# Performance work log

Measured on AMD Instinct MI355X. Metric: run time of the kernel, lower is better.

## Reference

```python
import jax, jax.numpy as jnp
import numpy as np

N = 50000      # nodes
E = 800000     # edges (avg degree 16)
IN = 100       # in_channels (hard-coded LayerNorm(100))
H = 128        # hidden_channels
G = 512        # num graphs in batch
C = 2          # num_classes
EPS = 1e-5     # LayerNorm eps (torch default)


def setup_inputs() -> dict:
    key = jax.random.key(0)
    ks = jax.random.split(key, 12)
    x = jax.random.normal(ks[0], (N, IN), dtype=jnp.float32)
    edge_index = jax.random.randint(ks[1], (2, E), 0, N, dtype=jnp.int64)
    edge_weight = jax.random.uniform(ks[2], (E,), dtype=jnp.float32)
    batch = jnp.sort(jax.random.randint(ks[3], (N,), 0, G, dtype=jnp.int64))
    # LayerNorm params (identity init, as torch)
    ln_g0, ln_b0 = jnp.ones((IN,), jnp.float32), jnp.zeros((IN,), jnp.float32)
    ln_g1, ln_b1 = jnp.ones((H,), jnp.float32), jnp.zeros((H,), jnp.float32)
    ln_g2, ln_b2 = jnp.ones((H,), jnp.float32), jnp.zeros((H,), jnp.float32)
    # GCNConv weights (glorot-ish scale) and biases
    W0 = jax.random.normal(ks[4], (IN, H), jnp.float32) / np.float32(np.sqrt(IN))
    b0 = jnp.zeros((H,), jnp.float32)
    W1 = jax.random.normal(ks[5], (H, H), jnp.float32) / np.float32(np.sqrt(H))
    b1 = jnp.zeros((H,), jnp.float32)
    W2 = jax.random.normal(ks[6], (H, H), jnp.float32) / np.float32(np.sqrt(H))
    b2 = jnp.zeros((H,), jnp.float32)
    # Final classifier
    Wlin = jax.random.normal(ks[7], (H, C), jnp.float32) / np.float32(np.sqrt(H))
    blin = jnp.zeros((C,), jnp.float32)
    return {"x": x, "edge_index": edge_index, "edge_weight": edge_weight,
            "batch": batch,
            "ln_g0": ln_g0, "ln_b0": ln_b0, "ln_g1": ln_g1, "ln_b1": ln_b1,
            "ln_g2": ln_g2, "ln_b2": ln_b2,
            "W0": W0, "b0": b0, "W1": W1, "b1": b1, "W2": W2, "b2": b2,
            "Wlin": Wlin, "blin": blin}


def _layernorm(h, g, b):
    m = jnp.mean(h, axis=-1, keepdims=True)
    v = jnp.mean(jnp.square(h - m), axis=-1, keepdims=True)
    return (h - m) * jax.lax.rsqrt(v + EPS) * g + b


def _gcn_conv(h, W, b, src, dst, edge_weight):
    # GCNConv(normalize=False): linear transform, edge gather scaled by
    # edge_weight, scatter-add to destination nodes, plus bias.
    hW = h @ W                                  # [N, H]
    msg = hW[src] * edge_weight[:, None]        # [E, H]
    agg = jax.ops.segment_sum(msg, dst, num_segments=N)  # [N, H]
    return agg + b


def reference(x, edge_index, edge_weight, batch,
              ln_g0, ln_b0, ln_g1, ln_b1, ln_g2, ln_b2,
              W0, b0, W1, b1, W2, b2, Wlin, blin):
    src, dst = edge_index[0], edge_index[1]
    layers = [(ln_g0, ln_b0, W0, b0), (ln_g1, ln_b1, W1, b1), (ln_g2, ln_b2, W2, b2)]
    h = x
    for (g, bb, W, cb) in layers:
        h = _layernorm(h, g, bb)
        h = _gcn_conv(h, W, cb, src, dst, edge_weight)
        h = jax.nn.relu(h)  # dropout is identity in eval mode
    # global mean pool over graphs
    sums = jax.ops.segment_sum(h, batch, num_segments=G)                       # [G, H]
    cnt = jax.ops.segment_sum(jnp.ones((N, 1), h.dtype), batch, num_segments=G)
    pooled = sums / jnp.maximum(cnt, 1.0)
    return pooled @ Wlin + blin  # [G, C]
```

## Files before the change

### kernel.cpp

```cpp
#include <hip/hip_runtime.h>
#include <hip/hip_bf16.h>

#define NN 50000
#define NE 800000
#define NG 512
#define HD 128
#define EPS 1e-5f
#define NB ((NN + 255) / 256)
#define L1B NB
#define EPB 4096
#define NL1 ((NE + EPB - 1) / EPB)

typedef __attribute__((ext_vector_type(8))) short short8;
typedef __attribute__((ext_vector_type(4))) float f32x4;

__global__ __launch_bounds__(256) void k_zero(int* __restrict__ deg,
                                              float* __restrict__ pooled) {
    const int i = blockIdx.x * 256 + threadIdx.x;
    if (i < NN) deg[i] = 0;
    if (i < NG * HD) pooled[i] = 0.f;
}

__global__ __launch_bounds__(256) void k_hist(const int* __restrict__ dstv,
                                              int* __restrict__ deg, int E) {
    int e = blockIdx.x * 256 + threadIdx.x;
    if (e < E) atomicAdd(&deg[dstv[e]], 1);
}

__global__ __launch_bounds__(256) void k_blksum(const int* __restrict__ deg,
                                                int* __restrict__ bsum) {
    __shared__ int red[4];
    const int i = blockIdx.x * 256 + threadIdx.x;
    int v = (i < NN) ? deg[i] : 0;
#pragma unroll
    for (int off = 32; off; off >>= 1) v += __shfl_down(v, off);
    const int lane = threadIdx.x & 63, w = threadIdx.x >> 6;
    if (lane == 0) red[w] = v;
    __syncthreads();
    if (threadIdx.x == 0) bsum[blockIdx.x] = red[0] + red[1] + red[2] + red[3];
}

__global__ __launch_bounds__(256) void k_scan_bsum(const int* __restrict__ bsum,
                                                   int* __restrict__ boff) {
    __shared__ int s[256];
    const int t = threadIdx.x;
    const int v = (t < NB) ? bsum[t] : 0;
    s[t] = v;
    __syncthreads();
    for (int off = 1; off < 256; off <<= 1) {
        int u = (t >= off) ? s[t - off] : 0;
        __syncthreads();
        s[t] += u;
        __syncthreads();
    }
    if (t < NB) boff[t] = s[t] - v;
}

__global__ __launch_bounds__(256) void k_scan_final(const int* __restrict__ deg,
                                                    const int* __restrict__ boff,
                                                    int* __restrict__ row_ptr) {
    __shared__ int s[256];
    const int t = threadIdx.x;
    const int i = blockIdx.x * 256 + t;
    const int v = (i < NN) ? deg[i] : 0;
    s[t] = v;
    __syncthreads();
    for (int off = 1; off < 256; off <<= 1) {
        int u = (t >= off) ? s[t - off] : 0;
        __syncthreads();
        s[t] += u;
        __syncthreads();
    }
    const int ex = boff[blockIdx.x] + s[t] - v;
    if (i < NN) row_ptr[i] = ex;
    if (i == NN - 1) row_ptr[NN] = ex + v;
}

__global__ __launch_bounds__(256) void k_initgc(const int* __restrict__ row_ptr,
                                                int* __restrict__ gcursor) {
    const int b = threadIdx.x;
    if (b < L1B) {
        int d = b << 8;
        gcursor[b] = row_ptr[(d < NN) ? d : NN];
    }
}

__global__ __launch_bounds__(256) void k_binL1(const int* __restrict__ srcv,
                                               const int* __restrict__ dstv,
                                               const float* __restrict__ ewt,
                                               int* __restrict__ gcursor,
                                               int2* __restrict__ stage, int E) {
    __shared__ int hist[L1B], lstart[L1B], gbase[L1B], lcur[L1B];
    __shared__ int s[256];
    __shared__ int2 lsort[EPB];
    const int t  = threadIdx.x;
    const int e0 = blockIdx.x * EPB;
    const int e1 = (e0 + EPB < E) ? (e0 + EPB) : E;
    for (int i = t; i < L1B; i += 256) hist[i] = 0;
    __syncthreads();
    for (int e = e0 + t; e < e1; e += 256)
        atomicAdd(&hist[dstv[e] >> 8], 1);
    __syncthreads();
    {
        const int v = (t < L1B) ? hist[t] : 0;
        s[t] = v;
        __syncthreads();
        for (int off = 1; off < 256; off <<= 1) {
            int u = (t >= off) ? s[t - off] : 0;
            __syncthreads();
            s[t] += u;
            __syncthreads();
        }
        if (t < L1B) {
            const int ex = s[t] - v;
            lstart[t] = ex;
            lcur[t]   = ex;
            gbase[t]  = v ? atomicAdd(&gcursor[t], v) : 0;
        }
    }
    __syncthreads();
    for (int e = e0 + t; e < e1; e += 256) {
        const int d = dstv[e];
        const int r = atomicAdd(&lcur[d >> 8], 1);
        lsort[r] = make_int2((d << 16) | srcv[e], __float_as_int(ewt[e]));
    }
    __syncthreads();
    const int n = e1 - e0;
    for (int i = t; i < n; i += 256) {
        const int2 el = lsort[i];
        const unsigned b = ((unsigned)el.x) >> 24;
        stage[gbase[b] + (i - lstart[b])] = el;
    }
}

__global__ __launch_bounds__(256) void k_binL2(const int2* __restrict__ stage,
                                               const int* __restrict__ row_ptr,
                                               int2* __restrict__ cw) {
    __shared__ int cur[256];
    const int t  = threadIdx.x;
    const int d0 = blockIdx.x << 8;
    const int nd = (NN - d0 < 256) ? (NN - d0) : 256;
    if (t < nd) cur[t] = row_ptr[d0 + t];
    __syncthreads();
    const int base = row_ptr[d0];
    const int end  = row_ptr[d0 + nd];
    for (int i = base + t; i < end; i += 256) {
        const int2 el = stage[i];
        const unsigned dst = ((unsigned)el.x) >> 16;
        const int p = atomicAdd(&cur[dst - d0], 1);
        cw[p] = make_int2(el.x & 0xFFFF, el.y);
    }
}

__global__ __launch_bounds__(256) void k_wpack(const float* __restrict__ W0,
                                               const float* __restrict__ W1,
                                               const float* __restrict__ W2,
                                               __hip_bfloat16* __restrict__ bp) {
    const int tg    = blockIdx.x * 256 + threadIdx.x;
    const int layer = tg >> 11;
    const int f     = tg & 2047;
    const int tile  = f >> 8, kk = (f >> 6) & 3, lane = f & 63;
    const int col   = tile * 16 + (lane & 15);
    const int kbase = kk * 32 + ((lane >> 4) << 3);
    const float* W  = (layer == 0) ? W0 : (layer == 1) ? W1 : W2;
    const int Klim  = (layer == 0) ? 100 : 128;
    alignas(16) __hip_bfloat16 o[8];
#pragma unroll
    for (int j = 0; j < 8; ++j) {
        const int k = kbase + j;
        o[j] = __float2bfloat16((k < Klim) ? W[(size_t)k * HD + col] : 0.f);
    }
    *(float4*)&bp[(size_t)tg * 8] = *(const float4*)o;
}

template <int K>
__global__ __launch_bounds__(256, 3) void k_ln_gemm(const float* __restrict__ hin,
                                                    const float* __restrict__ g,
                                                    const float* __restrict__ b,
                                                    const __hip_bfloat16* __restrict__ bp,
                                                    __hip_bfloat16* __restrict__ hwb) {
    constexpr int SK   = K + 4;
    constexpr int ROWS = 64;
    __shared__ float hs[ROWS][SK];
    __shared__ __hip_bfloat16 hb[ROWS][136];
    const int t  = threadIdx.x;
    const int r0 = blockIdx.x * ROWS;

    {
        const float4* src4 = (const float4*)(hin + (size_t)r0 * K);
        const int valid_rows = (NN - r0 < ROWS) ? (NN - r0) : ROWS;
        const int maxf = valid_rows * K;
        constexpr int NV = ROWS * K / 4;
        for (int i = t; i < NV; i += 256) {
            int f = i * 4;
            float4 v = (f < maxf) ? src4[i] : make_float4(0.f, 0.f, 0.f, 0.f);
            int r = f / K, k = f - r * K;
            *(float4*)&hs[r][k] = v;
        }
    }
    __syncthreads();

    {
        const int row = t >> 2, l = t & 3;
        float s = 0.f, s2 = 0.f;
        for (int k = l; k < K; k += 4) { float v = hs[row][k]; s += v; s2 += v * v; }
        s  += __shfl_xor(s, 1);  s2 += __shfl_xor(s2, 1);
        s  += __shfl_xor(s, 2);  s2 += __shfl_xor(s2, 2);
        const float mean = s / (float)K;
        const float var  = s2 / (float)K - mean * mean;
        const float rstd = rsqrtf(var + EPS);
        for (int k = l; k < K; k += 4)
            hb[row][k] = __float2bfloat16((hs[row][k] - mean) * rstd * g[k] + b[k]);
        for (int k = K + l; k < 128; k += 4)
            hb[row][k] = __float2bfloat16(0.f);
    }
    __syncthreads();

    const int wave = t >> 6, lane = t & 63;
    const int rw   = wave * 16;
    const int arow = rw + (lane & 15);
    const int acol = ((lane >> 4) << 3);
    short8 a[4];
#pragma unroll
    for (int kk = 0; kk < 4; ++kk)
        a[kk] = *(const short8*)&hb[arow][kk * 32 + acol];

    f32x4 acc[8] = {};
    const short8* bfr = (const short8*)bp;
#pragma unroll
    for (int tile = 0; tile < 8; ++tile) {
#pragma unroll
        for (int kk = 0; kk < 4; ++kk) {
            const short8 bb = bfr[(tile * 4 + kk) * 64 + lane];
            acc[tile] = __builtin_amdgcn_mfma_f32_16x16x32_bf16(a[kk], bb, acc[tile], 0, 0, 0);
        }
    }

    const int baser = r0 + rw + ((lane >> 4) << 2);
    const int bcol  = lane & 15;
#pragma unroll
    for (int tile = 0; tile < 8; ++tile) {
        const int col = tile * 16 + bcol;
#pragma unroll
        for (int j = 0; j < 4; ++j) {
            const int row = baser + j;
            if (row < NN) hwb[(size_t)row * HD + col] = __float2bfloat16(acc[tile][j]);
        }
    }
}

__device__ __forceinline__ float bfu(unsigned short u) {
    return __uint_as_float((unsigned)u << 16);
}

__device__ __forceinline__ float4 agg_row(const __hip_bfloat16* __restrict__ hwb,
                                          const int2* __restrict__ cw,
                                          const float* __restrict__ bias,
                                          int e0, int e1, size_t coff) {
    float4 acc = {0.f, 0.f, 0.f, 0.f};
    int e = e0;
    for (; e + 8 <= e1; e += 8) {
        int2 c[8];
#pragma unroll
        for (int j = 0; j < 8; ++j) c[j] = cw[e + j];
        ushort4 r[8];
#pragma unroll
        for (int j = 0; j < 8; ++j)
            r[j] = *(const ushort4*)(hwb + (size_t)c[j].x * HD + coff);
#pragma unroll
        for (int j = 0; j < 8; ++j) {
            const float w = __int_as_float(c[j].y);
            acc.x += w * bfu(r[j].x);
            acc.y += w * bfu(r[j].y);
            acc.z += w * bfu(r[j].z);
            acc.w += w * bfu(r[j].w);
        }
    }
    if (e + 4 <= e1) {
        int2 c[4];
#pragma unroll
        for (int j = 0; j < 4; ++j) c[j] = cw[e + j];
        ushort4 r[4];
#pragma unroll
        for (int j = 0; j < 4; ++j)
            r[j] = *(const ushort4*)(hwb + (size_t)c[j].x * HD + coff);
#pragma unroll
        for (int j = 0; j < 4; ++j) {
            const float w = __int_as_float(c[j].y);
            acc.x += w * bfu(r[j].x);
            acc.y += w * bfu(r[j].y);
            acc.z += w * bfu(r[j].z);
            acc.w += w * bfu(r[j].w);
        }
        e += 4;
    }
    for (; e < e1; ++e) {
        const int2 c = cw[e];
        const float w = __int_as_float(c.y);
        const ushort4 rv = *(const ushort4*)(hwb + (size_t)c.x * HD + coff);
        acc.x += w * bfu(rv.x);
        acc.y += w * bfu(rv.y);
        acc.z += w * bfu(rv.z);
        acc.w += w * bfu(rv.w);
    }
    const float4 bb = *(const float4*)(bias + coff);
    float4 o;
    o.x = fmaxf(acc.x + bb.x, 0.f);
    o.y = fmaxf(acc.y + bb.y, 0.f);
    o.z = fmaxf(acc.z + bb.z, 0.f);
    o.w = fmaxf(acc.w + bb.w, 0.f);
    return o;
}

__global__ __launch_bounds__(256) void k_aggregate(const __hip_bfloat16* __restrict__ hwb,
                                                   const int* __restrict__ row_ptr,
                                                   const int2* __restrict__ cw,
                                                   const float* __restrict__ bias,
                                                   float* __restrict__ hout, int n) {
    const int t    = threadIdx.x;
    const int grp  = t >> 5;
    const int lane = t & 31;
    const int node = blockIdx.x * 8 + grp;
    if (node >= n) return;
    const size_t coff = (size_t)lane * 4;
    float4 o = agg_row(hwb, cw, bias, row_ptr[node], row_ptr[node + 1], coff);
    *(float4*)(hout + (size_t)node * HD + coff) = o;
}

__global__ __launch_bounds__(256) void k_aggpool(const __hip_bfloat16* __restrict__ hwb,
                                                 const int* __restrict__ row_ptr,
                                                 const int2* __restrict__ cw,
                                                 const float* __restrict__ bias,
                                                 const int* __restrict__ batch,
                                                 float* __restrict__ pooled, int n) {
    __shared__ float lds[8][128];
    __shared__ int gof[8];
    const int t    = threadIdx.x;
    const int grp  = t >> 5;
    const int lane = t & 31;
    const int node = blockIdx.x * 8 + grp;
    const size_t coff = (size_t)lane * 4;
    float4 o = {0.f, 0.f, 0.f, 0.f};
    if (node < n)
        o = agg_row(hwb, cw, bias, row_ptr[node], row_ptr[node + 1], coff);
    *(float4*)&lds[grp][lane * 4] = o;
    if (lane == 0) gof[grp] = (node < n) ? batch[node] : -1;
    __syncthreads();
    if (t < 128) {
        float sum = 0.f;
        int curg = gof[0];
#pragma unroll
        for (int r = 0; r < 8; ++r) {
            const int gr = gof[r];
            if (gr != curg) {
                if (curg >= 0) atomicAdd(&pooled[curg * HD + t], sum);
                sum = 0.f;
                curg = gr;
            }
            if (gr >= 0) sum += lds[r][t];
        }
        if (curg >= 0) atomicAdd(&pooled[curg * HD + t], sum);
    }
}

__global__ __launch_bounds__(128) void k_linout(const float* __restrict__ pooled,
                                                const int* __restrict__ batch,
                                                const float* __restrict__ Wlin,
                                                const float* __restrict__ blin,
                                                float* __restrict__ out, int n) {
    __shared__ float red[2][128];
    const int gph = blockIdx.x;
    const int c   = threadIdx.x;
    int lo = 0, hi = n;
    while (lo < hi) { int mid = (lo + hi) >> 1; if (batch[mid] < gph) lo = mid + 1; else hi = mid; }
    const int start = lo;
    hi = n;
    while (lo < hi) { int mid = (lo + hi) >> 1; if (batch[mid] < gph + 1) lo = mid + 1; else hi = mid; }
    const float cnt = (float)(lo - start);
    const float pv = pooled[gph * HD + c] / fmaxf(cnt, 1.0f);
    red[0][c] = pv * Wlin[c * 2 + 0];
    red[1][c] = pv * Wlin[c * 2 + 1];
    __syncthreads();
    for (int off = 64; off; off >>= 1) {
        if (c < off) { red[0][c] += red[0][c + off]; red[1][c] += red[1][c + off]; }
        __syncthreads();
    }
    if (c == 0) {
        out[gph * 2 + 0] = red[0][0] + blin[0];
        out[gph * 2 + 1] = red[1][0] + blin[1];
    }
}

extern "C" void kernel_launch(void* const* d_in, const int* in_sizes, int n_in,
                              void* d_out, int out_size, void* d_ws, size_t ws_size,
                              hipStream_t stream) {
    const float* x     = (const float*)d_in[0];
    const int*   ei    = (const int*)d_in[1];
    const float* ewt   = (const float*)d_in[2];
    const int*   batch = (const int*)d_in[3];
    const float* ln_g0 = (const float*)d_in[4];
    const float* ln_b0 = (const float*)d_in[5];
    const float* ln_g1 = (const float*)d_in[6];
    const float* ln_b1 = (const float*)d_in[7];
    const float* ln_g2 = (const float*)d_in[8];
    const float* ln_b2 = (const float*)d_in[9];
    const float* W0    = (const float*)d_in[10];
    const float* b0    = (const float*)d_in[11];
    const float* W1    = (const float*)d_in[12];
    const float* b1    = (const float*)d_in[13];
    const float* W2    = (const float*)d_in[14];
    const float* b2    = (const float*)d_in[15];
    const float* Wlin  = (const float*)d_in[16];
    const float* blin  = (const float*)d_in[17];
    float* out = (float*)d_out;

    const int* srcv = ei;
    const int* dstv = ei + NE;

    char* ws = (char*)d_ws;
    size_t o = 0;
    auto carve = [&](size_t bytes) { void* p = ws + o; o += (bytes + 255) & ~(size_t)255; return p; };
    int*   deg     = (int*)carve(sizeof(int) * NN);
    int*   row_ptr = (int*)carve(sizeof(int) * (NN + 1));
    int*   gcursor = (int*)carve(sizeof(int) * L1B);
    int*   bsum    = (int*)carve(sizeof(int) * NB);
    int*   boff    = (int*)carve(sizeof(int) * NB);
    float* pooled  = (float*)carve(sizeof(float) * NG * HD);
    int2*  cw      = (int2*)carve(sizeof(int2) * NE);
    int2*  stage   = (int2*)carve(sizeof(int2) * NE);
    __hip_bfloat16* bpack = (__hip_bfloat16*)carve(sizeof(__hip_bfloat16) * 3 * 2048 * 8);
    __hip_bfloat16* hwb   = (__hip_bfloat16*)carve(sizeof(__hip_bfloat16) * NN * HD);
    float* hA      = (float*)carve(sizeof(float) * NN * HD);
    float* hB      = (float*)carve(sizeof(float) * NN * HD);
    (void)ws_size; (void)n_in; (void)in_sizes; (void)out_size;

    k_zero<<<256, 256, 0, stream>>>(deg, pooled);
    k_wpack<<<(3 * 2048) / 256, 256, 0, stream>>>(W0, W1, W2, bpack);

    k_hist<<<(NE + 255) / 256, 256, 0, stream>>>(dstv, deg, NE);
    k_blksum<<<NB, 256, 0, stream>>>(deg, bsum);
    k_scan_bsum<<<1, 256, 0, stream>>>(bsum, boff);
    k_scan_final<<<NB, 256, 0, stream>>>(deg, boff, row_ptr);
    k_initgc<<<1, 256, 0, stream>>>(row_ptr, gcursor);
    k_binL1<<<NL1, 256, 0, stream>>>(srcv, dstv, ewt, gcursor, stage, NE);
    k_binL2<<<NB, 256, 0, stream>>>(stage, row_ptr, cw);

    const int GEMM_GRID = (NN + 63) / 64;
    const int AGG_GRID  = (NN + 7) / 8;

    k_ln_gemm<100><<<GEMM_GRID, 256, 0, stream>>>(x, ln_g0, ln_b0, bpack, hwb);
    k_aggregate<<<AGG_GRID, 256, 0, stream>>>(hwb, row_ptr, cw, b0, hA, NN);
    k_ln_gemm<128><<<GEMM_GRID, 256, 0, stream>>>(hA, ln_g1, ln_b1, bpack + 2048 * 8, hwb);
    k_aggregate<<<AGG_GRID, 256, 0, stream>>>(hwb, row_ptr, cw, b1, hB, NN);
    k_ln_gemm<128><<<GEMM_GRID, 256, 0, stream>>>(hB, ln_g2, ln_b2, bpack + 2 * 2048 * 8, hwb);
    k_aggpool<<<AGG_GRID, 256, 0, stream>>>(hwb, row_ptr, cw, b2, batch, pooled, NN);
    k_linout<<<NG, 128, 0, stream>>>(pooled, batch, Wlin, blin, out, NN);
}
```

Before: 251.8 us.

## Build CSR from coarse bucket histogram and store hidden activations in bf16

The per-node degree histogram and its multi-kernel scan are replaced by a per-block histogram over 196 coarse buckets plus a single small scan. Each L2 binning block now derives row_ptr for its own 256 destinations with a local histogram and scan. Separately, the aggregate kernels write bf16 instead of fp32 activations, and a new bf16-input LayerNorm+GEMM kernel reads them, halving that intermediate traffic. The bf16 intermediates lower the precision of the LayerNorm inputs, and the L2 pass now reads its stage segment twice.

```diff
diff --git a/kernel.cpp b/kernel.cpp
--- a/kernel.cpp
+++ b/kernel.cpp
@@ -6,45 +6,45 @@
 #define NG 512
 #define HD 128
 #define EPS 1e-5f
-#define NB ((NN + 255) / 256)
-#define L1B NB
+#define L1B 196
 #define EPB 4096
 #define NL1 ((NE + EPB - 1) / EPB)
 
 typedef __attribute__((ext_vector_type(8))) short short8;
 typedef __attribute__((ext_vector_type(4))) float f32x4;
 
-__global__ __launch_bounds__(256) void k_zero(int* __restrict__ deg,
+__device__ __forceinline__ float bfu(unsigned short u) {
+    return __uint_as_float((unsigned)u << 16);
+}
+
+__global__ __launch_bounds__(256) void k_zero(int* __restrict__ gtot,
                                               float* __restrict__ pooled) {
     const int i = blockIdx.x * 256 + threadIdx.x;
-    if (i < NN) deg[i] = 0;
+    if (i < L1B) gtot[i] = 0;
     if (i < NG * HD) pooled[i] = 0.f;
 }
 
-__global__ __launch_bounds__(256) void k_hist(const int* __restrict__ dstv,
-                                              int* __restrict__ deg, int E) {
-    int e = blockIdx.x * 256 + threadIdx.x;
-    if (e < E) atomicAdd(&deg[dstv[e]], 1);
-}
-
-__global__ __launch_bounds__(256) void k_blksum(const int* __restrict__ deg,
-                                                int* __restrict__ bsum) {
-    __shared__ int red[4];
-    const int i = blockIdx.x * 256 + threadIdx.x;
-    int v = (i < NN) ? deg[i] : 0;
-#pragma unroll
-    for (int off = 32; off; off >>= 1) v += __shfl_down(v, off);
-    const int lane = threadIdx.x & 63, w = threadIdx.x >> 6;
-    if (lane == 0) red[w] = v;
-    __syncthreads();
-    if (threadIdx.x == 0) bsum[blockIdx.x] = red[0] + red[1] + red[2] + red[3];
-}
-
-__global__ __launch_bounds__(256) void k_scan_bsum(const int* __restrict__ bsum,
-                                                   int* __restrict__ boff) {
+__global__ __launch_bounds__(256) void k_histL1(const int* __restrict__ dstv,
+                                                int* __restrict__ gtot, int E) {
+    __shared__ int h[L1B];
+    const int t  = threadIdx.x;
+    const int e0 = blockIdx.x * EPB;
+    const int e1 = (e0 + EPB < E) ? (e0 + EPB) : E;
+    for (int i = t; i < L1B; i += 256) h[i] = 0;
+    __syncthreads();
+    for (int e = e0 + t; e < e1; e += 256) atomicAdd(&h[dstv[e] >> 8], 1);
+    __syncthreads();
+    for (int i = t; i < L1B; i += 256)
+        if (h[i]) atomicAdd(&gtot[i], h[i]);
+}
+
+__global__ __launch_bounds__(256) void k_scan196(const int* __restrict__ gtot,
+                                                 int* __restrict__ gbase,
+                                                 int* __restrict__ gcursor,
+                                                 int* __restrict__ row_ptr) {
     __shared__ int s[256];
     const int t = threadIdx.x;
-    const int v = (t < NB) ? bsum[t] : 0;
+    const int v = (t < L1B) ? gtot[t] : 0;
     s[t] = v;
     __syncthreads();
     for (int off = 1; off < 256; off <<= 1) {
@@ -53,36 +53,9 @@
         s[t] += u;
         __syncthreads();
     }
-    if (t < NB) boff[t] = s[t] - v;
-}
-
-__global__ __launch_bounds__(256) void k_scan_final(const int* __restrict__ deg,
-                                                    const int* __restrict__ boff,
-                                                    int* __restrict__ row_ptr) {
-    __shared__ int s[256];
-    const int t = threadIdx.x;
-    const int i = blockIdx.x * 256 + t;
-    const int v = (i < NN) ? deg[i] : 0;
-    s[t] = v;
-    __syncthreads();
-    for (int off = 1; off < 256; off <<= 1) {
-        int u = (t >= off) ? s[t - off] : 0;
-        __syncthreads();
-        s[t] += u;
-        __syncthreads();
-    }
-    const int ex = boff[blockIdx.x] + s[t] - v;
-    if (i < NN) row_ptr[i] = ex;
-    if (i == NN - 1) row_ptr[NN] = ex + v;
-}
-
-__global__ __launch_bounds__(256) void k_initgc(const int* __restrict__ row_ptr,
-                                                int* __restrict__ gcursor) {
-    const int b = threadIdx.x;
-    if (b < L1B) {
-        int d = b << 8;
-        gcursor[b] = row_ptr[(d < NN) ? d : NN];
-    }
+    const int ex = s[t] - v;
+    if (t < L1B) { gbase[t] = ex; gcursor[t] = ex; }
+    if (t == 0) { gbase[L1B] = NE; row_ptr[NN] = NE; }
 }
 
 __global__ __launch_bounds__(256) void k_binL1(const int* __restrict__ srcv,
@@ -134,16 +107,38 @@
 }
 
 __global__ __launch_bounds__(256) void k_binL2(const int2* __restrict__ stage,
-                                               const int* __restrict__ row_ptr,
+                                               const int* __restrict__ gbase,
+                                               int* __restrict__ row_ptr,
                                                int2* __restrict__ cw) {
-    __shared__ int cur[256];
-    const int t  = threadIdx.x;
-    const int d0 = blockIdx.x << 8;
-    const int nd = (NN - d0 < 256) ? (NN - d0) : 256;
-    if (t < nd) cur[t] = row_ptr[d0 + t];
-    __syncthreads();
-    const int base = row_ptr[d0];
-    const int end  = row_ptr[d0 + nd];
+    __shared__ int cnt[256], s[256], cur[256];
+    const int t    = threadIdx.x;
+    const int b    = blockIdx.x;
+    const int d0   = b << 8;
+    const int nd   = (NN - d0 < 256) ? (NN - d0) : 256;
+    const int base = gbase[b];
+    const int end  = gbase[b + 1];
+    cnt[t] = 0;
+    __syncthreads();
+    for (int i = base + t; i < end; i += 256) {
+        const unsigned dst = ((unsigned)stage[i].x) >> 16;
+        atomicAdd(&cnt[dst - d0], 1);
+    }
+    __syncthreads();
+    {
+        const int v = cnt[t];
+        s[t] = v;
+        __syncthreads();
+        for (int off = 1; off < 256; off <<= 1) {
+            int u = (t >= off) ? s[t - off] : 0;
+            __syncthreads();
+            s[t] += u;
+            __syncthreads();
+        }
+        const int ex = base + s[t] - v;
+        cur[t] = ex;
+        if (t < nd) row_ptr[d0 + t] = ex;
+    }
+    __syncthreads();
     for (int i = base + t; i < end; i += 256) {
         const int2 el = stage[i];
         const unsigned dst = ((unsigned)el.x) >> 16;
@@ -173,25 +168,58 @@
     *(float4*)&bp[(size_t)tg * 8] = *(const float4*)o;
 }
 
-template <int K>
-__global__ __launch_bounds__(256, 3) void k_ln_gemm(const float* __restrict__ hin,
-                                                    const float* __restrict__ g,
-                                                    const float* __restrict__ b,
-                                                    const __hip_bfloat16* __restrict__ bp,
-                                                    __hip_bfloat16* __restrict__ hwb) {
-    constexpr int SK   = K + 4;
-    constexpr int ROWS = 64;
-    __shared__ float hs[ROWS][SK];
-    __shared__ __hip_bfloat16 hb[ROWS][136];
+__device__ __forceinline__ void mfma_gemm_store(const __hip_bfloat16 (*hb)[136],
+                                                const __hip_bfloat16* __restrict__ bp,
+                                                __hip_bfloat16* __restrict__ hwb,
+                                                int t, int r0) {
+    const int wave = t >> 6, lane = t & 63;
+    const int rw   = wave * 16;
+    const int arow = rw + (lane & 15);
+    const int acol = ((lane >> 4) << 3);
+    short8 a[4];
+#pragma unroll
+    for (int kk = 0; kk < 4; ++kk)
+        a[kk] = *(const short8*)&hb[arow][kk * 32 + acol];
+
+    f32x4 acc[8] = {};
+    const short8* bfr = (const short8*)bp;
+#pragma unroll
+    for (int tile = 0; tile < 8; ++tile) {
+#pragma unroll
+        for (int kk = 0; kk < 4; ++kk) {
+            const short8 bb = bfr[(tile * 4 + kk) * 64 + lane];
+            acc[tile] = __builtin_amdgcn_mfma_f32_16x16x32_bf16(a[kk], bb, acc[tile], 0, 0, 0);
+        }
+    }
+    const int baser = r0 + rw + ((lane >> 4) << 2);
+    const int bcol  = lane & 15;
+#pragma unroll
+    for (int tile = 0; tile < 8; ++tile) {
+        const int col = tile * 16 + bcol;
+#pragma unroll
+        for (int j = 0; j < 4; ++j) {
+            const int row = baser + j;
+            if (row < NN) hwb[(size_t)row * HD + col] = __float2bfloat16(acc[tile][j]);
+        }
+    }
+}
+
+__global__ __launch_bounds__(256, 3) void k_ln_gemm_f32(const float* __restrict__ hin,
+                                                        const float* __restrict__ g,
+                                                        const float* __restrict__ b,
+                                                        const __hip_bfloat16* __restrict__ bp,
+                                                        __hip_bfloat16* __restrict__ hwb) {
+    constexpr int K  = 100;
+    constexpr int SK = K + 4;
+    __shared__ float hs[64][SK];
+    __shared__ __hip_bfloat16 hb[64][136];
     const int t  = threadIdx.x;
-    const int r0 = blockIdx.x * ROWS;
-
+    const int r0 = blockIdx.x * 64;
     {
         const float4* src4 = (const float4*)(hin + (size_t)r0 * K);
-        const int valid_rows = (NN - r0 < ROWS) ? (NN - r0) : ROWS;
+        const int valid_rows = (NN - r0 < 64) ? (NN - r0) : 64;
         const int maxf = valid_rows * K;
-        constexpr int NV = ROWS * K / 4;
-        for (int i = t; i < NV; i += 256) {
+        for (int i = t; i < 64 * K / 4; i += 256) {
             int f = i * 4;
             float4 v = (f < maxf) ? src4[i] : make_float4(0.f, 0.f, 0.f, 0.f);
             int r = f / K, k = f - r * K;
@@ -199,7 +227,6 @@
         }
     }
     __syncthreads();
-
     {
         const int row = t >> 2, l = t & 3;
         float s = 0.f, s2 = 0.f;
@@ -215,42 +242,45 @@
             hb[row][k] = __float2bfloat16(0.f);
     }
     __syncthreads();
-
-    const int wave = t >> 6, lane = t & 63;
-    const int rw   = wave * 16;
-    const int arow = rw + (lane & 15);
-    const int acol = ((lane >> 4) << 3);
-    short8 a[4];
-#pragma unroll
-    for (int kk = 0; kk < 4; ++kk)
-        a[kk] = *(const short8*)&hb[arow][kk * 32 + acol];
-
-    f32x4 acc[8] = {};
-    const short8* bfr = (const short8*)bp;
-#pragma unroll
-    for (int tile = 0; tile < 8; ++tile) {
-#pragma unroll
-        for (int kk = 0; kk < 4; ++kk) {
-            const short8 bb = bfr[(tile * 4 + kk) * 64 + lane];
-            acc[tile] = __builtin_amdgcn_mfma_f32_16x16x32_bf16(a[kk], bb, acc[tile], 0, 0, 0);
-        }
-    }
-
-    const int baser = r0 + rw + ((lane >> 4) << 2);
-    const int bcol  = lane & 15;
-#pragma unroll
-    for (int tile = 0; tile < 8; ++tile) {
-        const int col = tile * 16 + bcol;
-#pragma unroll
-        for (int j = 0; j < 4; ++j) {
-            const int row = baser + j;
-            if (row < NN) hwb[(size_t)row * HD + col] = __float2bfloat16(acc[tile][j]);
-        }
-    }
-}
-
-__device__ __forceinline__ float bfu(unsigned short u) {
-    return __uint_as_float((unsigned)u << 16);
+    mfma_gemm_store(hb, bp, hwb, t, r0);
+}
+
+__global__ __launch_bounds__(256, 4) void k_ln_gemm_b16(const __hip_bfloat16* __restrict__ hin,
+                                                        const float* __restrict__ g,
+                                                        const float* __restrict__ b,
+                                                        const __hip_bfloat16* __restrict__ bp,
+                                                        __hip_bfloat16* __restrict__ hwb) {
+    __shared__ __hip_bfloat16 hb[64][136];
+    const int t  = threadIdx.x;
+    const int r0 = blockIdx.x * 64;
+    {
+        const float4* src4 = (const float4*)(hin + (size_t)r0 * HD);
+        const int valid_rows = (NN - r0 < 64) ? (NN - r0) : 64;
+        const int maxv = valid_rows * 16;
+        for (int i = t; i < 1024; i += 256) {
+            float4 v = (i < maxv) ? src4[i] : make_float4(0.f, 0.f, 0.f, 0.f);
+            const int r = i >> 4, k = (i & 15) * 8;
+            *(float4*)&hb[r][k] = v;
+        }
+    }
+    __syncthreads();
+    {
+        const int row = t >> 2, l = t & 3;
+        float s = 0.f, s2 = 0.f;
+        for (int k = l; k < 128; k += 4) {
+            const float v = __bfloat162float(hb[row][k]);
+            s += v; s2 += v * v;
+        }
+        s  += __shfl_xor(s, 1);  s2 += __shfl_xor(s2, 1);
+        s  += __shfl_xor(s, 2);  s2 += __shfl_xor(s2, 2);
+        const float mean = s / 128.f;
+        const float var  = s2 / 128.f - mean * mean;
+        const float rstd = rsqrtf(var + EPS);
+        for (int k = l; k < 128; k += 4)
+            hb[row][k] = __float2bfloat16((__bfloat162float(hb[row][k]) - mean) * rstd * g[k] + b[k]);
+    }
+    __syncthreads();
+    mfma_gemm_store(hb, bp, hwb, t, r0);
 }
 
 __device__ __forceinline__ float4 agg_row(const __hip_bfloat16* __restrict__ hwb,
@@ -316,7 +346,7 @@
                                                    const int* __restrict__ row_ptr,
                                                    const int2* __restrict__ cw,
                                                    const float* __restrict__ bias,
-                                                   float* __restrict__ hout, int n) {
+                                                   __hip_bfloat16* __restrict__ hout, int n) {
     const int t    = threadIdx.x;
     const int grp  = t >> 5;
     const int lane = t & 31;
@@ -324,7 +354,10 @@
     if (node >= n) return;
     const size_t coff = (size_t)lane * 4;
     float4 o = agg_row(hwb, cw, bias, row_ptr[node], row_ptr[node + 1], coff);
-    *(float4*)(hout + (size_t)node * HD + coff) = o;
+    alignas(8) __hip_bfloat16 ob[4] = {
+        __float2bfloat16(o.x), __float2bfloat16(o.y),
+        __float2bfloat16(o.z), __float2bfloat16(o.w)};
+    *(ushort4*)(hout + (size_t)node * HD + coff) = *(const ushort4*)ob;
 }
 
 __global__ __launch_bounds__(256) void k_aggpool(const __hip_bfloat16* __restrict__ hwb,
@@ -420,39 +453,35 @@
     char* ws = (char*)d_ws;
     size_t o = 0;
     auto carve = [&](size_t bytes) { void* p = ws + o; o += (bytes + 255) & ~(size_t)255; return p; };
-    int*   deg     = (int*)carve(sizeof(int) * NN);
     int*   row_ptr = (int*)carve(sizeof(int) * (NN + 1));
+    int*   gtot    = (int*)carve(sizeof(int) * L1B);
+    int*   gbase   = (int*)carve(sizeof(int) * (L1B + 1));
     int*   gcursor = (int*)carve(sizeof(int) * L1B);
-    int*   bsum    = (int*)carve(sizeof(int) * NB);
-    int*   boff    = (int*)carve(sizeof(int) * NB);
     float* pooled  = (float*)carve(sizeof(float) * NG * HD);
     int2*  cw      = (int2*)carve(sizeof(int2) * NE);
     int2*  stage   = (int2*)carve(sizeof(int2) * NE);
     __hip_bfloat16* bpack = (__hip_bfloat16*)carve(sizeof(__hip_bfloat16) * 3 * 2048 * 8);
     __hip_bfloat16* hwb   = (__hip_bfloat16*)carve(sizeof(__hip_bfloat16) * NN * HD);
-    float* hA      = (float*)carve(sizeof(float) * NN * HD);
-    float* hB      = (float*)carve(sizeof(float) * NN * HD);
+    __hip_bfloat16* hA    = (__hip_bfloat16*)carve(sizeof(__hip_bfloat16) * NN * HD);
+    __hip_bfloat16* hB    = (__hip_bfloat16*)carve(sizeof(__hip_bfloat16) * NN * HD);
     (void)ws_size; (void)n_in; (void)in_sizes; (void)out_size;
 
-    k_zero<<<256, 256, 0, stream>>>(deg, pooled);
+    k_zero<<<256, 256, 0, stream>>>(gtot, pooled);
     k_wpack<<<(3 * 2048) / 256, 256, 0, stream>>>(W0, W1, W2, bpack);
 
-    k_hist<<<(NE + 255) / 256, 256, 0, stream>>>(dstv, deg, NE);
-    k_blksum<<<NB, 256, 0, stream>>>(deg, bsum);
-    k_scan_bsum<<<1, 256, 0, stream>>>(bsum, boff);
-    k_scan_final<<<NB, 256, 0, stream>>>(deg, boff, row_ptr);
-    k_initgc<<<1, 256, 0, stream>>>(row_ptr, gcursor);
+    k_histL1<<<NL1, 256, 0, stream>>>(dstv, gtot, NE);
+    k_scan196<<<1, 256, 0, stream>>>(gtot, gbase, gcursor, row_ptr);
     k_binL1<<<NL1, 256, 0, stream>>>(srcv, dstv, ewt, gcursor, stage, NE);
-    k_binL2<<<NB, 256, 0, stream>>>(stage, row_ptr, cw);
+    k_binL2<<<L1B, 256, 0, stream>>>(stage, gbase, row_ptr, cw);
 
     const int GEMM_GRID = (NN + 63) / 64;
     const int AGG_GRID  = (NN + 7) / 8;
 
-    k_ln_gemm<100><<<GEMM_GRID, 256, 0, stream>>>(x, ln_g0, ln_b0, bpack, hwb);
+    k_ln_gemm_f32<<<GEMM_GRID, 256, 0, stream>>>(x, ln_g0, ln_b0, bpack, hwb);
     k_aggregate<<<AGG_GRID, 256, 0, stream>>>(hwb, row_ptr, cw, b0, hA, NN);
-    k_ln_gemm<128><<<GEMM_GRID, 256, 0, stream>>>(hA, ln_g1, ln_b1, bpack + 2048 * 8, hwb);
+    k_ln_gemm_b16<<<GEMM_GRID, 256, 0, stream>>>(hA, ln_g1, ln_b1, bpack + 2048 * 8, hwb);
     k_aggregate<<<AGG_GRID, 256, 0, stream>>>(hwb, row_ptr, cw, b1, hB, NN);
-    k_ln_gemm<128><<<GEMM_GRID, 256, 0, stream>>>(hB, ln_g2, ln_b2, bpack + 2 * 2048 * 8, hwb);
+    k_ln_gemm_b16<<<GEMM_GRID, 256, 0, stream>>>(hB, ln_g2, ln_b2, bpack + 2 * 2048 * 8, hwb);
     k_aggpool<<<AGG_GRID, 256, 0, stream>>>(hwb, row_ptr, cw, b2, batch, pooled, NN);
     k_linout<<<NG, 128, 0, stream>>>(pooled, batch, Wlin, blin, out, NN);
 }
```

Result: faster. 210.9 us (-16.2%).
